# Kernel optimization log

Hardware: AMD Instinct MI355X
Metric: run time of the kernel (lower is better)

## Reference

```python
import jax, jax.numpy as jnp
import numpy as np

B, D_IN, D_BOT, C = 8192, 2048, 1024, 1000
SHARE = 500          # cfg.share_class_num
TEMP = 0.05          # cfg.temp
NEG_FILL = -1e9
EPS = 1e-12          # F.normalize eps


def setup_inputs() -> dict:
    key = jax.random.key(0)
    ks = jax.random.split(key, 6)
    return {
        "features": jax.random.normal(ks[0], (B, D_IN), jnp.float32),
        "W_b": jax.random.normal(ks[1], (D_BOT, D_IN), jnp.float32) * 0.02,
        "b_b": jnp.zeros((D_BOT,), jnp.float32),
        "W1": jax.random.normal(ks[2], (C, D_BOT), jnp.float32) * 0.02,
        "W2": jax.random.normal(ks[3], (C, D_BOT), jnp.float32) * 0.02,
        "centroid": jax.random.normal(ks[4], (C, D_BOT), jnp.float32) * 0.02,
    }


def mask_mechanism(outputs):
    # per-row mask: argmax -> row mask -> masked softmax (branchless)
    predict = jnp.argmax(outputs, axis=1)                       # [B]
    cls = jnp.arange(C)                                          # [C]
    base = cls < SHARE                                           # shared classes masked
    # if predicted class is private (>= SHARE), mask the whole row ...
    row_mask = jnp.where((predict >= SHARE)[:, None], True, base[None, :])
    # ... but always unmask the predicted class itself
    row_mask = row_mask & (cls[None, :] != predict[:, None])     # [B, C] bool
    masked = jnp.where(row_mask, jnp.float32(NEG_FILL), outputs)
    return jax.nn.softmax(masked, axis=1)


def reference(features, W_b, b_b, W1, W2, centroid):
    feats = features @ W_b.T + b_b                               # bottleneck [B, D_BOT]
    outputs1 = feats @ W1.T                                      # [B, C]
    sm1 = mask_mechanism(outputs1)
    feat_oa = sm1 @ centroid                                     # [B, D_BOT]
    features_aug = feats + feat_oa
    # F.normalize(dim=1): x / max(||x||_2, eps)
    norm = jnp.sqrt(jnp.sum(features_aug * features_aug, axis=1, keepdims=True))
    x = features_aug / jnp.maximum(norm, EPS)
    outputs2 = (x @ W2.T) / TEMP                                 # [B, C]
    softmax_outputs = jax.nn.softmax(outputs2, axis=1)
    return (feats, features_aug, outputs1, outputs2, softmax_outputs)
```

## Files before the change

kernel.cpp:

```cpp
#include <hip/hip_runtime.h>
#include <cmath>


typedef _Float16 h8 __attribute__((ext_vector_type(8)));
typedef _Float16 h4 __attribute__((ext_vector_type(4)));
typedef float f32x4 __attribute__((ext_vector_type(4)));

#define TAU 0.010f
#define CAP 1024

__device__ __forceinline__ void gload_lds16(const _Float16* g, _Float16* l) {
    __builtin_amdgcn_global_load_lds(
        (const __attribute__((address_space(1))) void*)g,
        (__attribute__((address_space(3))) void*)l, 16, 0, 0);
}

__device__ __forceinline__ void split4(f32x4 v, h4& h, h4& l) {
    #pragma unroll
    for (int j = 0; j < 4; ++j) {
        _Float16 hh = (_Float16)v[j];
        h[j] = hh;
        l[j] = (_Float16)((v[j] - (float)hh) * 2048.0f);
    }
}

__global__ __launch_bounds__(256) void prep_kernel(
    const float* __restrict__ features, _Float16* __restrict__ fh,
    const float* __restrict__ W_b, _Float16* __restrict__ wbh, _Float16* __restrict__ wbl,
    const float* __restrict__ W1, _Float16* __restrict__ w1h, _Float16* __restrict__ w1l,
    const float* __restrict__ W2, _Float16* __restrict__ w2h,
    const float* __restrict__ centroid, _Float16* __restrict__ cth,
    int* __restrict__ cnt)
{
    __shared__ float tile[32][33];
    const int bid = blockIdx.x;
    const int t = threadIdx.x;
    if (bid == 0 && t == 0) *cnt = 0;

    if (bid < 2048) {
        for (int i = bid * 256 + t; i < 4194304; i += 2048 * 256) {
            f32x4 v = ((const f32x4*)features)[i];
            h4 h;
            #pragma unroll
            for (int j = 0; j < 4; ++j) h[j] = (_Float16)v[j];
            ((h4*)fh)[i] = h;
        }
    } else if (bid < 3072) {
        const int i = (bid - 2048) * 512 + t;
        #pragma unroll
        for (int q = 0; q < 2; ++q) {
            const int k = i + q * 256;
            f32x4 v = ((const f32x4*)W_b)[k];
            h4 h, l; split4(v, h, l);
            ((h4*)wbh)[k] = h;
            ((h4*)wbl)[k] = l;
        }
    } else if (bid < 4096) {
        const int i = (bid - 3072) * 256 + t;
        const int r = i >> 8;
        f32x4 v = {0.f, 0.f, 0.f, 0.f};
        if (r < 1000) v = ((const f32x4*)W1)[i];
        h4 h, l; split4(v, h, l);
        ((h4*)w1h)[i] = h;
        ((h4*)w1l)[i] = l;
    } else if (bid < 5120) {
        const int local = bid - 4096;
        const int n0 = (local & 31) * 32, k0 = (local >> 5) * 32;
        const int tx = t & 31, ty = t >> 5;
        #pragma unroll
        for (int p = 0; p < 4; ++p) {
            int k = k0 + ty + p * 8;
            tile[ty + p * 8][tx] = (k < 1000) ? centroid[(size_t)k * 1024 + n0 + tx] : 0.0f;
        }
        __syncthreads();
        #pragma unroll
        for (int p = 0; p < 4; ++p) {
            int n = n0 + ty + p * 8;
            cth[(size_t)n * 1024 + k0 + tx] = (_Float16)tile[tx][ty + p * 8];
        }
    } else {
        const int i = (bid - 5120) * 256 + t;
        const int r = i >> 8;
        f32x4 v = {0.f, 0.f, 0.f, 0.f};
        if (r < 1000) v = ((const f32x4*)W2)[i];
        h4 h;
        #pragma unroll
        for (int j = 0; j < 4; ++j) h[j] = (_Float16)v[j];
        ((h4*)w2h)[i] = h;
    }
}

template <int MODE>
__global__ __launch_bounds__(256, 4) void gemm16(
    const _Float16* __restrict__ Ah, int lda,
    const _Float16* __restrict__ Bh, int ldb, int K,
    float* __restrict__ C, int ldc, int nC,
    const float* __restrict__ aux, _Float16* __restrict__ Ch)
{
    __shared__ _Float16 sAh[128 * 64];
    __shared__ _Float16 sBh[128 * 64];

    const int t = threadIdx.x;
    const int lane = t & 63, wid = t >> 6;
    const int wg = blockIdx.x;
    const int wgid = (wg & 7) * 64 + (wg >> 3);
    const int row0 = (wgid >> 3) * 128, col0 = (wgid & 7) * 128;
    const int wr = wid >> 1, wc = wid & 1;
    const int fr = lane & 15;
    const int fk = (lane >> 4) * 8;
    const int srow = lane >> 3;
    const int scol = (lane & 7) * 8;

    f32x4 acc[4][4] = {};

    for (int k0 = 0; k0 < K; k0 += 64) {
        #pragma unroll
        for (int j = 0; j < 4; ++j) {
            int i = wid * 4 + j;
            int r = i * 8 + srow;
            gload_lds16(Ah + (size_t)(row0 + r) * lda + k0 + scol, &sAh[i * 512]);
            gload_lds16(Bh + (size_t)(col0 + r) * ldb + k0 + scol, &sBh[i * 512]);
        }
        __syncthreads();
        #pragma unroll
        for (int ks = 0; ks < 2; ++ks) {
            h8 ah[4];
            #pragma unroll
            for (int mf = 0; mf < 4; ++mf)
                ah[mf] = *(const h8*)&sAh[(wr * 64 + mf * 16 + fr) * 64 + ks * 32 + fk];
            #pragma unroll
            for (int nf = 0; nf < 4; ++nf) {
                h8 bh = *(const h8*)&sBh[(wc * 64 + nf * 16 + fr) * 64 + ks * 32 + fk];
                #pragma unroll
                for (int mf = 0; mf < 4; ++mf)
                    acc[mf][nf] = __builtin_amdgcn_mfma_f32_16x16x32_f16(ah[mf], bh, acc[mf][nf], 0, 0, 0);
            }
        }
        __syncthreads();
    }
    #pragma unroll
    for (int mf = 0; mf < 4; ++mf) {
        #pragma unroll
        for (int nf = 0; nf < 4; ++nf) {
            f32x4 v = acc[mf][nf];
            const int gcol = col0 + wc * 64 + nf * 16 + fr;
            const int rbase = row0 + wr * 64 + mf * 16 + (lane >> 4) * 4;
            #pragma unroll
            for (int j = 0; j < 4; ++j) {
                const int grow = rbase + j;
                float val = v[j];
                if constexpr (MODE == 1) val += aux[gcol];
                if constexpr (MODE == 3) val += aux[(size_t)grow * 1024 + gcol];
                if constexpr (MODE == 4) val *= 20.0f;
                if (gcol < nC) {
                    C[(size_t)grow * ldc + gcol] = val;
                    if constexpr (MODE == 1)
                        Ch[(size_t)grow * 1024 + gcol] = (_Float16)val;
                }
            }
        }
    }
}

__global__ __launch_bounds__(256, 2) void gemmc(
    const _Float16* __restrict__ Ah, const _Float16* __restrict__ Al, int lda,
    const _Float16* __restrict__ Bh, const _Float16* __restrict__ Bl, int ldb,
    int klen,
    float* __restrict__ C, int ldc, int nC,
    const int* __restrict__ cnt)
{
    __shared__ _Float16 sAh[128 * 64];
    __shared__ _Float16 sBh[128 * 64];
    __shared__ _Float16 sAl[128 * 64];
    __shared__ _Float16 sBl[128 * 64];

    const int t = threadIdx.x;
    const int lane = t & 63, wid = t >> 6;
    const int row0 = blockIdx.y * 128, col0 = blockIdx.x * 128;
    const int kbase = blockIdx.z * klen;
    if (row0 >= *cnt) return;
    const int wr = wid >> 1, wc = wid & 1;
    const int fr = lane & 15;
    const int fk = (lane >> 4) * 8;
    const int srow = lane >> 3;
    const int scol = (lane & 7) * 8;

    f32x4 acc[4][4] = {};
    f32x4 accc[4][4] = {};

    for (int k0 = kbase; k0 < kbase + klen; k0 += 64) {
        #pragma unroll
        for (int j = 0; j < 4; ++j) {
            int i = wid * 4 + j;
            int r = i * 8 + srow;
            const size_t ga = (size_t)(row0 + r) * lda + k0 + scol;
            const size_t gb = (size_t)(col0 + r) * ldb + k0 + scol;
            gload_lds16(Ah + ga, &sAh[i * 512]);
            gload_lds16(Bh + gb, &sBh[i * 512]);
            gload_lds16(Al + ga, &sAl[i * 512]);
            gload_lds16(Bl + gb, &sBl[i * 512]);
        }
        __syncthreads();
        #pragma unroll
        for (int ks = 0; ks < 2; ++ks) {
            h8 ah[4], al[4];
            #pragma unroll
            for (int mf = 0; mf < 4; ++mf) {
                int rr = wr * 64 + mf * 16 + fr;
                ah[mf] = *(const h8*)&sAh[rr * 64 + ks * 32 + fk];
                al[mf] = *(const h8*)&sAl[rr * 64 + ks * 32 + fk];
            }
            #pragma unroll
            for (int nf = 0; nf < 4; ++nf) {
                int cc = wc * 64 + nf * 16 + fr;
                h8 bh = *(const h8*)&sBh[cc * 64 + ks * 32 + fk];
                h8 bl = *(const h8*)&sBl[cc * 64 + ks * 32 + fk];
                #pragma unroll
                for (int mf = 0; mf < 4; ++mf) {
                    acc[mf][nf]  = __builtin_amdgcn_mfma_f32_16x16x32_f16(ah[mf], bh, acc[mf][nf], 0, 0, 0);
                    accc[mf][nf] = __builtin_amdgcn_mfma_f32_16x16x32_f16(ah[mf], bl, accc[mf][nf], 0, 0, 0);
                    accc[mf][nf] = __builtin_amdgcn_mfma_f32_16x16x32_f16(al[mf], bh, accc[mf][nf], 0, 0, 0);
                }
            }
        }
        __syncthreads();
    }
    float* Cz = C + (size_t)blockIdx.z * CAP * ldc;
    #pragma unroll
    for (int mf = 0; mf < 4; ++mf) {
        #pragma unroll
        for (int nf = 0; nf < 4; ++nf) {
            f32x4 v = acc[mf][nf] + accc[mf][nf] * (1.0f / 2048.0f);
            const int gcol = col0 + wc * 64 + nf * 16 + fr;
            const int rbase = row0 + wr * 64 + mf * 16 + (lane >> 4) * 4;
            #pragma unroll
            for (int j = 0; j < 4; ++j) {
                if (gcol < nC) Cz[(size_t)(rbase + j) * ldc + gcol] = v[j];
            }
        }
    }
}

__device__ __forceinline__ void masked_softmax_body(
    const float* __restrict__ x, _Float16* __restrict__ y,
    int t, float* wv, int* wi, bool flag, int* d_idx, int* d_cnt, int rowid,
    int* s_slot)
{
    float bv = -1e30f, sv = -1e30f; int bi = 0;
    for (int c = t; c < 1000; c += 256) {
        float v = x[c];
        if (v > bv) { sv = bv; bv = v; bi = c; }
        else if (v > sv) sv = v;
    }
    #pragma unroll
    for (int off = 32; off > 0; off >>= 1) {
        float ov = __shfl_down(bv, off, 64);
        int   oi = __shfl_down(bi, off, 64);
        float os = __shfl_down(sv, off, 64);
        if (ov > bv || (ov == bv && oi < bi)) {
            sv = fmaxf(bv, os); bv = ov; bi = oi;
        } else {
            sv = fmaxf(sv, fmaxf(ov, os) == ov ? ov : os);
            sv = fmaxf(sv, ov); sv = fmaxf(sv, os);
        }
    }
    __shared__ float svv[4];
    const int lane = t & 63, wid = t >> 6;
    if (lane == 0) { wv[wid] = bv; wi[wid] = bi; svv[wid] = sv; }
    __syncthreads();
    __shared__ float s_m, s_tot; __shared__ int s_p;
    if (t == 0) {
        float mv = wv[0]; int mi = wi[0]; float m2 = svv[0];
        for (int w = 1; w < 4; ++w) {
            if (wv[w] > mv || (wv[w] == mv && wi[w] < mi)) {
                m2 = fmaxf(mv, svv[w]); mv = wv[w]; mi = wi[w];
            } else {
                m2 = fmaxf(m2, fmaxf(wv[w], svv[w]));
            }
        }
        s_p = mi; s_m = mv;
        int slot = -1;
        if (flag && (mv - m2) < TAU) {
            int q = atomicAdd(d_cnt, 1);
            if (q < CAP) { d_idx[q] = rowid; slot = q; }
        }
        *s_slot = slot;
    }
    __syncthreads();
    const int p = s_p; const float m = s_m;
    if (p >= 500) {
        for (int c = t; c < 1024; c += 256) y[c] = (c == p) ? (_Float16)1.0f : (_Float16)0.0f;
    } else {
        float s = 0.f;
        for (int c = t; c < 1000; c += 256)
            if (c == p || c >= 500) s += expf(x[c] - m);
        #pragma unroll
        for (int off = 32; off > 0; off >>= 1) s += __shfl_down(s, off, 64);
        if (lane == 0) wv[wid] = s;
        __syncthreads();
        if (t == 0) s_tot = wv[0] + wv[1] + wv[2] + wv[3];
        __syncthreads();
        const float inv = 1.0f / s_tot;
        for (int c = t; c < 1024; c += 256) {
            float v = 0.f;
            if (c < 1000 && (c == p || c >= 500)) v = expf(x[c] - m) * inv;
            y[c] = (_Float16)v;
        }
    }
}

__global__ __launch_bounds__(256) void masksm_kernel(
    const float* __restrict__ o1, _Float16* __restrict__ sm,
    const float* __restrict__ features,
    _Float16* __restrict__ fgh, _Float16* __restrict__ fgl,
    int* __restrict__ d_idx, int* __restrict__ d_cnt)
{
    __shared__ float wv[4]; __shared__ int wi[4]; __shared__ int s_slot;
    const int row = blockIdx.x;
    const int t = threadIdx.x;
    masked_softmax_body(o1 + (size_t)row * 1000, sm + (size_t)row * 1024,
                        t, wv, wi, true, d_idx, d_cnt, row, &s_slot);
    const int slot = s_slot;
    if (slot >= 0) {
        #pragma unroll
        for (int q = 0; q < 2; ++q) {
            int o = t * 8 + q * 4;
            f32x4 v = *(const f32x4*)(features + (size_t)row * 2048 + o);
            h4 h, l; split4(v, h, l);
            *(h4*)(fgh + (size_t)slot * 2048 + o) = h;
            *(h4*)(fgl + (size_t)slot * 2048 + o) = l;
        }
    }
}

__global__ __launch_bounds__(256) void fixup_kernel(const float* __restrict__ P2,
                                                    _Float16* __restrict__ sm,
                                                    const int* __restrict__ d_idx,
                                                    const int* __restrict__ d_cnt)
{
    const int slot = blockIdx.x;
    if (slot >= *d_cnt || slot >= CAP) return;
    const int row = d_idx[slot];
    const int t = threadIdx.x;
    __shared__ float xr[1000];
    for (int c = t; c < 1000; c += 256) {
        const size_t o = (size_t)slot * 1000 + c;
        xr[c] = P2[o] + P2[o + (size_t)CAP * 1000];
    }
    __syncthreads();
    __shared__ float wv[4]; __shared__ int wi[4]; __shared__ int s_slot;
    masked_softmax_body(xr, sm + (size_t)row * 1024,
                        t, wv, wi, false, nullptr, nullptr, 0, &s_slot);
}

__global__ __launch_bounds__(256) void red1_kernel(const float* __restrict__ P1,
                                                   const float* __restrict__ bias,
                                                   _Float16* __restrict__ fgsh,
                                                   _Float16* __restrict__ fgsl,
                                                   const int* __restrict__ d_cnt)
{
    const int slot = blockIdx.x;
    if (slot >= *d_cnt || slot >= CAP) return;
    const int t = threadIdx.x;
    #pragma unroll
    for (int q = 0; q < 4; ++q) {
        const int c = t + q * 256;
        const size_t o = (size_t)slot * 1024 + c;
        float s = P1[o] + P1[o + (size_t)CAP * 1024] + P1[o + (size_t)2 * CAP * 1024]
                + P1[o + (size_t)3 * CAP * 1024] + bias[c];
        _Float16 h = (_Float16)s;
        fgsh[o] = h;
        fgsl[o] = (_Float16)((s - (float)h) * 2048.0f);
    }
}

__global__ __launch_bounds__(256) void rownorm_x_kernel(const float* __restrict__ aug,
                                                        _Float16* __restrict__ xh)
{
    const int row = blockIdx.x; const int t = threadIdx.x;
    f32x4 v = *((const f32x4*)(aug + (size_t)row * 1024) + t);
    float s = v[0]*v[0] + v[1]*v[1] + v[2]*v[2] + v[3]*v[3];
    #pragma unroll
    for (int off = 32; off > 0; off >>= 1) s += __shfl_down(s, off, 64);
    __shared__ float ws4[4]; __shared__ float s_inv;
    const int lane = t & 63, wid = t >> 6;
    if (lane == 0) ws4[wid] = s;
    __syncthreads();
    if (t == 0) {
        float tot = ws4[0] + ws4[1] + ws4[2] + ws4[3];
        s_inv = 1.0f / fmaxf(sqrtf(tot), 1e-12f);
    }
    __syncthreads();
    const float inv = s_inv;
    h4 h;
    #pragma unroll
    for (int j = 0; j < 4; ++j) h[j] = (_Float16)(v[j] * inv);
    *((h4*)(xh + (size_t)row * 1024) + t) = h;
}

__global__ __launch_bounds__(256) void softmax2_kernel(const float* __restrict__ o2,
                                                       float* __restrict__ out)
{
    const int row = blockIdx.x; const int t = threadIdx.x;
    const float* x = o2 + (size_t)row * 1000;
    float* y = out + (size_t)row * 1000;
    float m = -1e30f;
    for (int c = t; c < 1000; c += 256) m = fmaxf(m, x[c]);
    #pragma unroll
    for (int off = 32; off > 0; off >>= 1) m = fmaxf(m, __shfl_down(m, off, 64));
    __shared__ float sm4[4]; __shared__ float s_m, s_s;
    const int lane = t & 63, wid = t >> 6;
    if (lane == 0) sm4[wid] = m;
    __syncthreads();
    if (t == 0) s_m = fmaxf(fmaxf(sm4[0], sm4[1]), fmaxf(sm4[2], sm4[3]));
    __syncthreads();
    m = s_m;
    float s = 0.f;
    for (int c = t; c < 1000; c += 256) s += expf(x[c] - m);
    #pragma unroll
    for (int off = 32; off > 0; off >>= 1) s += __shfl_down(s, off, 64);
    if (lane == 0) sm4[wid] = s;
    __syncthreads();
    if (t == 0) s_s = sm4[0] + sm4[1] + sm4[2] + sm4[3];
    __syncthreads();
    const float inv = 1.0f / s_s;
    for (int c = t; c < 1000; c += 256) y[c] = expf(x[c] - m) * inv;
}

extern "C" void kernel_launch(void* const* d_in, const int* in_sizes, int n_in,
                              void* d_out, int out_size, void* d_ws, size_t ws_size,
                              hipStream_t stream)
{
    const float* features = (const float*)d_in[0];
    const float* W_b      = (const float*)d_in[1];
    const float* b_b      = (const float*)d_in[2];
    const float* W1       = (const float*)d_in[3];
    const float* W2       = (const float*)d_in[4];
    const float* centroid = (const float*)d_in[5];

    char* base = (char*)d_out;
    float* feats = (float*)(base);
    float* aug   = (float*)(base + 33554432);
    float* o1    = (float*)(base + 67108864);
    float* o2    = (float*)(base + 99876864);
    float* smx   = (float*)(base + 132644864);

    _Float16* fh    = (_Float16*)(base + 67108864);
    _Float16* fetsh = (_Float16*)(base + 33554432);
    float*    P1    = (float*)   (base + 33554432);
    float*    P2    = (float*)   (base + 33554432);
    int*      idx   = (int*)     (base + 50331648);
    int*      cnt   = (int*)     (base + 50339840);
    _Float16* fgsh  = (_Float16*)(base + 50348032);
    _Float16* fgsl  = (_Float16*)(base + 52445184);
    _Float16* sm1h  = (_Float16*)(base + 99876864);
    _Float16* cth   = (_Float16*)(base + 116654080);
    _Float16* wbh   = (_Float16*)(base + 118751232);
    _Float16* wbl   = (_Float16*)(base + 122945536);
    _Float16* w2h   = (_Float16*)(base + 132644864);
    _Float16* w1h   = (_Float16*)(base + 142606336);
    _Float16* w1l   = (_Float16*)(base + 144703488);
    _Float16* fgh   = (_Float16*)(base + 146800640);
    _Float16* fgl   = (_Float16*)(base + 150994944);
    _Float16* xh    = (_Float16*)(base + 146800640);

    prep_kernel<<<6144, 256, 0, stream>>>(features, fh, W_b, wbh, wbl,
                                          W1, w1h, w1l, W2, w2h, centroid, cth, cnt);
    gemm16<1><<<512, 256, 0, stream>>>(fh, 2048, wbh, 2048, 2048,
                                       feats, 1024, 1024, b_b, fetsh);
    gemm16<2><<<512, 256, 0, stream>>>(fetsh, 1024, w1h, 1024, 1024,
                                       o1, 1000, 1000, nullptr, nullptr);
    masksm_kernel<<<8192, 256, 0, stream>>>(o1, sm1h, features, fgh, fgl, idx, cnt);
    gemmc<<<dim3(8, CAP / 128, 4), 256, 0, stream>>>(fgh, fgl, 2048, wbh, wbl, 2048, 512,
                                                     P1, 1024, 1024, cnt);
    red1_kernel<<<CAP, 256, 0, stream>>>(P1, b_b, fgsh, fgsl, cnt);
    gemmc<<<dim3(8, CAP / 128, 2), 256, 0, stream>>>(fgsh, fgsl, 1024, w1h, w1l, 1024, 512,
                                                     P2, 1000, 1000, cnt);
    fixup_kernel<<<CAP, 256, 0, stream>>>(P2, sm1h, idx, cnt);
    gemm16<3><<<512, 256, 0, stream>>>(sm1h, 1024, cth, 1024, 1024,
                                       aug, 1024, 1024, feats, nullptr);
    rownorm_x_kernel<<<8192, 256, 0, stream>>>(aug, xh);
    gemm16<4><<<512, 256, 0, stream>>>(xh, 1024, w2h, 1024, 1024,
                                       o2, 1000, 1000, nullptr, nullptr);
    softmax2_kernel<<<8192, 256, 0, stream>>>(o2, smx);
}
```

Measured before the change: 288.3 us.

## Exploit mask sparsity: halve centroid GEMM K, add predicted-class term in epilogue

The masked softmax is nonzero only on private classes 500..999 plus the predicted class. The sm1 @ centroid GEMM now runs with K=512 over the private-class centroids only, and the predicted class's weight and index are stored per row and added in the epilogue as a rank-1 gather from the fp32 centroid. This roughly halves that GEMM's work and the transposed-centroid prep, at the cost of an extra gathered load per output element. It also caches logits in LDS for the masked softmax, splits the correction GEMM into four K-slices, and keeps softmax2 values in registers instead of reloading them.

```diff
diff --git a/kernel.cpp b/kernel.cpp
--- a/kernel.cpp
+++ b/kernel.cpp
@@ -29,7 +29,7 @@
     const float* __restrict__ W_b, _Float16* __restrict__ wbh, _Float16* __restrict__ wbl,
     const float* __restrict__ W1, _Float16* __restrict__ w1h, _Float16* __restrict__ w1l,
     const float* __restrict__ W2, _Float16* __restrict__ w2h,
-    const float* __restrict__ centroid, _Float16* __restrict__ cth,
+    const float* __restrict__ centroid, _Float16* __restrict__ cthc,
     int* __restrict__ cnt)
 {
     __shared__ float tile[32][33];
@@ -63,23 +63,23 @@
         h4 h, l; split4(v, h, l);
         ((h4*)w1h)[i] = h;
         ((h4*)w1l)[i] = l;
-    } else if (bid < 5120) {
+    } else if (bid < 4608) {
         const int local = bid - 4096;
         const int n0 = (local & 31) * 32, k0 = (local >> 5) * 32;
         const int tx = t & 31, ty = t >> 5;
         #pragma unroll
         for (int p = 0; p < 4; ++p) {
             int k = k0 + ty + p * 8;
-            tile[ty + p * 8][tx] = (k < 1000) ? centroid[(size_t)k * 1024 + n0 + tx] : 0.0f;
+            tile[ty + p * 8][tx] = (k < 500) ? centroid[(size_t)(500 + k) * 1024 + n0 + tx] : 0.0f;
         }
         __syncthreads();
         #pragma unroll
         for (int p = 0; p < 4; ++p) {
             int n = n0 + ty + p * 8;
-            cth[(size_t)n * 1024 + k0 + tx] = (_Float16)tile[tx][ty + p * 8];
+            cthc[(size_t)n * 512 + k0 + tx] = (_Float16)tile[tx][ty + p * 8];
         }
     } else {
-        const int i = (bid - 5120) * 256 + t;
+        const int i = (bid - 4608) * 256 + t;
         const int r = i >> 8;
         f32x4 v = {0.f, 0.f, 0.f, 0.f};
         if (r < 1000) v = ((const f32x4*)W2)[i];
@@ -95,7 +95,9 @@
     const _Float16* __restrict__ Ah, int lda,
     const _Float16* __restrict__ Bh, int ldb, int K,
     float* __restrict__ C, int ldc, int nC,
-    const float* __restrict__ aux, _Float16* __restrict__ Ch)
+    const float* __restrict__ aux, _Float16* __restrict__ Ch,
+    const float* __restrict__ cent, const int* __restrict__ pidx,
+    const float* __restrict__ pw)
 {
     __shared__ _Float16 sAh[128 * 64];
     __shared__ _Float16 sBh[128 * 64];
@@ -150,7 +152,11 @@
                 const int grow = rbase + j;
                 float val = v[j];
                 if constexpr (MODE == 1) val += aux[gcol];
-                if constexpr (MODE == 3) val += aux[(size_t)grow * 1024 + gcol];
+                if constexpr (MODE == 3) {
+                    const int p = pidx[grow];
+                    val += aux[(size_t)grow * 1024 + gcol]
+                         + pw[grow] * cent[(size_t)p * 1024 + gcol];
+                }
                 if constexpr (MODE == 4) val *= 20.0f;
                 if (gcol < nC) {
                     C[(size_t)grow * ldc + gcol] = val;
@@ -243,6 +249,7 @@
 
 __device__ __forceinline__ void masked_softmax_body(
     const float* __restrict__ x, _Float16* __restrict__ y,
+    float* __restrict__ pwp, int* __restrict__ pidxp,
     int t, float* wv, int* wi, bool flag, int* d_idx, int* d_cnt, int rowid,
     int* s_slot)
 {
@@ -289,7 +296,8 @@
     __syncthreads();
     const int p = s_p; const float m = s_m;
     if (p >= 500) {
-        for (int c = t; c < 1024; c += 256) y[c] = (c == p) ? (_Float16)1.0f : (_Float16)0.0f;
+        for (int c = t; c < 512; c += 256) y[c] = (_Float16)0.0f;
+        if (t == 0) { pwp[0] = 1.0f; pidxp[0] = p; }
     } else {
         float s = 0.f;
         for (int c = t; c < 1000; c += 256)
@@ -301,24 +309,30 @@
         if (t == 0) s_tot = wv[0] + wv[1] + wv[2] + wv[3];
         __syncthreads();
         const float inv = 1.0f / s_tot;
-        for (int c = t; c < 1024; c += 256) {
+        for (int c = t; c < 512; c += 256) {
             float v = 0.f;
-            if (c < 1000 && (c == p || c >= 500)) v = expf(x[c] - m) * inv;
+            if (c < 500) v = expf(x[500 + c] - m) * inv;
             y[c] = (_Float16)v;
         }
+        if (t == 0) { pwp[0] = inv; pidxp[0] = p; }
     }
 }
 
 __global__ __launch_bounds__(256) void masksm_kernel(
-    const float* __restrict__ o1, _Float16* __restrict__ sm,
+    const float* __restrict__ o1, _Float16* __restrict__ sm1c,
+    float* __restrict__ pwa, int* __restrict__ pidxa,
     const float* __restrict__ features,
     _Float16* __restrict__ fgh, _Float16* __restrict__ fgl,
     int* __restrict__ d_idx, int* __restrict__ d_cnt)
 {
+    __shared__ float xs[1000];
     __shared__ float wv[4]; __shared__ int wi[4]; __shared__ int s_slot;
     const int row = blockIdx.x;
     const int t = threadIdx.x;
-    masked_softmax_body(o1 + (size_t)row * 1000, sm + (size_t)row * 1024,
+    const float* x = o1 + (size_t)row * 1000;
+    for (int c = t; c < 1000; c += 256) xs[c] = x[c];
+    __syncthreads();
+    masked_softmax_body(xs, sm1c + (size_t)row * 512, pwa + row, pidxa + row,
                         t, wv, wi, true, d_idx, d_cnt, row, &s_slot);
     const int slot = s_slot;
     if (slot >= 0) {
@@ -333,10 +347,10 @@
     }
 }
 
-__global__ __launch_bounds__(256) void fixup_kernel(const float* __restrict__ P2,
-                                                    _Float16* __restrict__ sm,
-                                                    const int* __restrict__ d_idx,
-                                                    const int* __restrict__ d_cnt)
+__global__ __launch_bounds__(256) void fixup_kernel(
+    const float* __restrict__ P2, _Float16* __restrict__ sm1c,
+    float* __restrict__ pwa, int* __restrict__ pidxa,
+    const int* __restrict__ d_idx, const int* __restrict__ d_cnt)
 {
     const int slot = blockIdx.x;
     if (slot >= *d_cnt || slot >= CAP) return;
@@ -345,11 +359,12 @@
     __shared__ float xr[1000];
     for (int c = t; c < 1000; c += 256) {
         const size_t o = (size_t)slot * 1000 + c;
-        xr[c] = P2[o] + P2[o + (size_t)CAP * 1000];
+        xr[c] = (P2[o] + P2[o + (size_t)CAP * 1000])
+              + (P2[o + (size_t)2 * CAP * 1000] + P2[o + (size_t)3 * CAP * 1000]);
     }
     __syncthreads();
     __shared__ float wv[4]; __shared__ int wi[4]; __shared__ int s_slot;
-    masked_softmax_body(xr, sm + (size_t)row * 1024,
+    masked_softmax_body(xr, sm1c + (size_t)row * 512, pwa + row, pidxa + row,
                         t, wv, wi, false, nullptr, nullptr, 0, &s_slot);
 }
 
@@ -404,8 +419,10 @@
     const int row = blockIdx.x; const int t = threadIdx.x;
     const float* x = o2 + (size_t)row * 1000;
     float* y = out + (size_t)row * 1000;
-    float m = -1e30f;
-    for (int c = t; c < 1000; c += 256) m = fmaxf(m, x[c]);
+    const bool has3 = (t < 232);
+    float v0 = x[t], v1 = x[t + 256], v2 = x[t + 512];
+    float v3 = has3 ? x[t + 768] : -1e30f;
+    float m = fmaxf(fmaxf(v0, v1), fmaxf(v2, v3));
     #pragma unroll
     for (int off = 32; off > 0; off >>= 1) m = fmaxf(m, __shfl_down(m, off, 64));
     __shared__ float sm4[4]; __shared__ float s_m, s_s;
@@ -415,8 +432,9 @@
     if (t == 0) s_m = fmaxf(fmaxf(sm4[0], sm4[1]), fmaxf(sm4[2], sm4[3]));
     __syncthreads();
     m = s_m;
-    float s = 0.f;
-    for (int c = t; c < 1000; c += 256) s += expf(x[c] - m);
+    float e0 = expf(v0 - m), e1 = expf(v1 - m), e2 = expf(v2 - m);
+    float e3 = has3 ? expf(v3 - m) : 0.0f;
+    float s = (e0 + e1) + (e2 + e3);
     #pragma unroll
     for (int off = 32; off > 0; off >>= 1) s += __shfl_down(s, off, 64);
     if (lane == 0) sm4[wid] = s;
@@ -424,7 +442,10 @@
     if (t == 0) s_s = sm4[0] + sm4[1] + sm4[2] + sm4[3];
     __syncthreads();
     const float inv = 1.0f / s_s;
-    for (int c = t; c < 1000; c += 256) y[c] = expf(x[c] - m) * inv;
+    y[t] = e0 * inv;
+    y[t + 256] = e1 * inv;
+    y[t + 512] = e2 * inv;
+    if (has3) y[t + 768] = e3 * inv;
 }
 
 extern "C" void kernel_launch(void* const* d_in, const int* in_sizes, int n_in,
@@ -453,8 +474,10 @@
     int*      cnt   = (int*)     (base + 50339840);
     _Float16* fgsh  = (_Float16*)(base + 50348032);
     _Float16* fgsl  = (_Float16*)(base + 52445184);
-    _Float16* sm1h  = (_Float16*)(base + 99876864);
-    _Float16* cth   = (_Float16*)(base + 116654080);
+    _Float16* sm1c  = (_Float16*)(base + 99876864);
+    int*      pidx  = (int*)     (base + 108265472);
+    float*    pw    = (float*)   (base + 108298240);
+    _Float16* cthc  = (_Float16*)(base + 116654080);
     _Float16* wbh   = (_Float16*)(base + 118751232);
     _Float16* wbl   = (_Float16*)(base + 122945536);
     _Float16* w2h   = (_Float16*)(base + 132644864);
@@ -464,23 +487,28 @@
     _Float16* fgl   = (_Float16*)(base + 150994944);
     _Float16* xh    = (_Float16*)(base + 146800640);
 
-    prep_kernel<<<6144, 256, 0, stream>>>(features, fh, W_b, wbh, wbl,
-                                          W1, w1h, w1l, W2, w2h, centroid, cth, cnt);
+    prep_kernel<<<5632, 256, 0, stream>>>(features, fh, W_b, wbh, wbl,
+                                          W1, w1h, w1l, W2, w2h, centroid, cthc, cnt);
     gemm16<1><<<512, 256, 0, stream>>>(fh, 2048, wbh, 2048, 2048,
-                                       feats, 1024, 1024, b_b, fetsh);
+                                       feats, 1024, 1024, b_b, fetsh,
+                                       nullptr, nullptr, nullptr);
     gemm16<2><<<512, 256, 0, stream>>>(fetsh, 1024, w1h, 1024, 1024,
-                                       o1, 1000, 1000, nullptr, nullptr);
-    masksm_kernel<<<8192, 256, 0, stream>>>(o1, sm1h, features, fgh, fgl, idx, cnt);
+                                       o1, 1000, 1000, nullptr, nullptr,
+                                       nullptr, nullptr, nullptr);
+    masksm_kernel<<<8192, 256, 0, stream>>>(o1, sm1c, pw, pidx, features,
+                                            fgh, fgl, idx, cnt);
     gemmc<<<dim3(8, CAP / 128, 4), 256, 0, stream>>>(fgh, fgl, 2048, wbh, wbl, 2048, 512,
                                                      P1, 1024, 1024, cnt);
     red1_kernel<<<CAP, 256, 0, stream>>>(P1, b_b, fgsh, fgsl, cnt);
-    gemmc<<<dim3(8, CAP / 128, 2), 256, 0, stream>>>(fgsh, fgsl, 1024, w1h, w1l, 1024, 512,
+    gemmc<<<dim3(8, CAP / 128, 4), 256, 0, stream>>>(fgsh, fgsl, 1024, w1h, w1l, 1024, 256,
                                                      P2, 1000, 1000, cnt);
-    fixup_kernel<<<CAP, 256, 0, stream>>>(P2, sm1h, idx, cnt);
-    gemm16<3><<<512, 256, 0, stream>>>(sm1h, 1024, cth, 1024, 1024,
-                                       aug, 1024, 1024, feats, nullptr);
+    fixup_kernel<<<CAP, 256, 0, stream>>>(P2, sm1c, pw, pidx, idx, cnt);
+    gemm16<3><<<512, 256, 0, stream>>>(sm1c, 512, cthc, 512, 512,
+                                       aug, 1024, 1024, feats, nullptr,
+                                       centroid, pidx, pw);
     rownorm_x_kernel<<<8192, 256, 0, stream>>>(aug, xh);
     gemm16<4><<<512, 256, 0, stream>>>(xh, 1024, w2h, 1024, 1024,
-                                       o2, 1000, 1000, nullptr, nullptr);
+                                       o2, 1000, 1000, nullptr, nullptr,
+                                       nullptr, nullptr, nullptr);
     softmax2_kernel<<<8192, 256, 0, stream>>>(o2, smx);
 }
```

Result: faster. 260.2 us (-9.8%).
